# Performance work log

Measured on AMD Instinct MI355X. Metric: run time of the kernel, lower is better.

The kernel has to match this reference:

```python
import jax, jax.numpy as jnp
import numpy as np


def gin_conv(x, src, dst, W, b, num_nodes):
    # PyG GINConv with eps=0: nn((1+eps)*x + sum_{j in N(i)} x_j)
    agg = jax.ops.segment_sum(x[src], dst, num_segments=num_nodes)
    return (x + agg) @ W + b


def setup_inputs() -> dict:
    key = jax.random.key(0)
    ks = jax.random.split(key, 16)
    N, E, F, G = 100000, 3200000, 64, 512
    x = jax.random.normal(ks[0], (N, F), dtype=jnp.float32)
    edge_index = jax.random.randint(ks[1], (2, E), 0, N, dtype=jnp.int64)
    batch = jnp.sort(jax.random.randint(ks[2], (N,), 0, G, dtype=jnp.int64))

    def lin(k, fi, fo):
        return jax.random.normal(k, (fi, fo), dtype=jnp.float32) / np.sqrt(fi)

    return {
        "x": x, "edge_index": edge_index, "batch": batch, "num_graphs": G,
        "W1": lin(ks[3], F, 32), "b1": jnp.zeros((32,), jnp.float32),
        "W2": lin(ks[4], 32, 64), "b2": jnp.zeros((64,), jnp.float32),
        "W3": lin(ks[5], 64, 64), "b3": jnp.zeros((64,), jnp.float32),
        "Wf1": lin(ks[6], 64, 64), "bf1": jnp.zeros((64,), jnp.float32),
        "Wf2": lin(ks[7], 64, 32), "bf2": jnp.zeros((32,), jnp.float32),
        "Wf3": lin(ks[8], 32, 1), "bf3": jnp.zeros((1,), jnp.float32),
    }


def reference(x, edge_index, batch, num_graphs,
              W1, b1, W2, b2, W3, b3, Wf1, bf1, Wf2, bf2, Wf3, bf3):
    N = x.shape[0]
    src, dst = edge_index[0], edge_index[1]
    h = jax.nn.elu(gin_conv(x, src, dst, W1, b1, N))
    h = jax.nn.elu(gin_conv(h, src, dst, W2, b2, N))
    h = jax.nn.elu(gin_conv(h, src, dst, W3, b3, N))
    # scatter_mean pooling over graphs
    sums = jax.ops.segment_sum(h, batch, num_segments=num_graphs)
    cnts = jax.ops.segment_sum(jnp.ones((N,), h.dtype), batch, num_segments=num_graphs)
    g = sums / jnp.maximum(cnts, 1.0)[:, None]
    g = jax.nn.elu(g @ Wf1 + bf1)
    g = jax.nn.elu(g @ Wf2 + bf2)
    g = g @ Wf3 + bf3
    return g.reshape(-1)
```

## Files before the change

kernel.cpp:

```cpp
#include <hip/hip_runtime.h>
#include <hip/hip_bf16.h>


typedef float f4 __attribute__((ext_vector_type(4)));

#define NCHUNK 512
#define MAXK 1024

__device__ __forceinline__ float elu_f(float x) {
  return x > 0.0f ? x : expm1f(x);
}

__device__ __forceinline__ float rl(float v, int q) {
  return __int_as_float(__builtin_amdgcn_readlane(__float_as_int(v), q));
}

__device__ __forceinline__ unsigned short f2bf(float f) {
  unsigned int u = __float_as_uint(f);
  u = (u + 0x7FFFu + ((u >> 16) & 1u)) >> 16;
  return (unsigned short)u;
}

__device__ __forceinline__ void acc_add8(float* a, const uint4 w) {
  a[0] += __uint_as_float(w.x << 16);
  a[1] += __uint_as_float(w.x & 0xffff0000u);
  a[2] += __uint_as_float(w.y << 16);
  a[3] += __uint_as_float(w.y & 0xffff0000u);
  a[4] += __uint_as_float(w.z << 16);
  a[5] += __uint_as_float(w.z & 0xffff0000u);
  a[6] += __uint_as_float(w.w << 16);
  a[7] += __uint_as_float(w.w & 0xffff0000u);
}


__global__ __launch_bounds__(256) void cvt_bf16_kernel(
    const float* __restrict__ in, unsigned short* __restrict__ out, int n4) {
  typedef unsigned short us4 __attribute__((ext_vector_type(4)));
  const int stride = gridDim.x * blockDim.x;
  for (int i = blockIdx.x * blockDim.x + threadIdx.x; i < n4; i += stride) {
    const f4 v = *reinterpret_cast<const f4*>(in + (long long)i * 4);
    us4 o;
    o.x = f2bf(v.x); o.y = f2bf(v.y); o.z = f2bf(v.z); o.w = f2bf(v.w);
    *reinterpret_cast<us4*>(out + (long long)i * 4) = o;
  }
}


__global__ __launch_bounds__(256) void bucket_hist_kernel(
    const int* __restrict__ dst, int* __restrict__ bhist, int E, int K, int chunk) {
  __shared__ int h[MAXK];
  for (int k = threadIdx.x; k < K; k += 256) h[k] = 0;
  __syncthreads();
  const int base = blockIdx.x * chunk;
  const int end = min(E, base + chunk);
  for (int e = base + threadIdx.x; e < end; e += 256)
    atomicAdd(&h[dst[e] >> 7], 1);
  __syncthreads();
  int* row = bhist + (long long)blockIdx.x * K;
  for (int k = threadIdx.x; k < K; k += 256) row[k] = h[k];
}

__global__ __launch_bounds__(NCHUNK) void chunk_scan_kernel(
    const int* __restrict__ bhist, int* __restrict__ cursors,
    int* __restrict__ btot, int K) {
  __shared__ int s[NCHUNK];
  const int k = blockIdx.x;
  const int t = threadIdx.x;
  const int own = bhist[(long long)t * K + k];
  s[t] = own;
  __syncthreads();
#pragma unroll
  for (int off = 1; off < NCHUNK; off <<= 1) {
    int v = (t >= off) ? s[t - off] : 0;
    __syncthreads();
    s[t] += v;
    __syncthreads();
  }
  cursors[(long long)t * K + k] = s[t] - own;
  if (t == NCHUNK - 1) btot[k] = s[t];
}

__global__ __launch_bounds__(1024) void bucket_scan_kernel(
    const int* __restrict__ btot, int* __restrict__ bstart, int K) {
  __shared__ int s[1024];
  const int t = threadIdx.x;
  const int own = (t < K) ? btot[t] : 0;
  s[t] = own;
  __syncthreads();
#pragma unroll
  for (int off = 1; off < 1024; off <<= 1) {
    int v = (t >= off) ? s[t - off] : 0;
    __syncthreads();
    s[t] += v;
    __syncthreads();
  }
  if (t < K) bstart[t] = s[t] - own;
  if (t == K - 1) bstart[K] = s[t];
}

__global__ __launch_bounds__(256) void bucket_scatter_kernel(
    const int* __restrict__ src, const int* __restrict__ dst,
    const int* __restrict__ cursors, const int* __restrict__ bstart,
    int* __restrict__ packed, int E, int K, int chunk) {
  __shared__ int cur[MAXK];
  const int c = blockIdx.x;
  for (int k = threadIdx.x; k < K; k += 256)
    cur[k] = cursors[(long long)c * K + k] + bstart[k];
  __syncthreads();
  const int base = c * chunk;
  const int end = min(E, base + chunk);
  for (int e = base + threadIdx.x; e < end; e += 256) {
    const int d = dst[e];
    const int k = d >> 7;
    const int p = atomicAdd(&cur[k], 1);
    packed[p] = ((d & 127) << 18) | src[e];
  }
}

__global__ __launch_bounds__(256) void bucket_sort_kernel(
    const int* __restrict__ packed, const int* __restrict__ bstart,
    int* __restrict__ rowptr, int* __restrict__ eidx, int N, int E, int K) {
  __shared__ int hcnt[128];
  __shared__ int sc[128];
  __shared__ int ccur[128];
  const int k = blockIdx.x;
  const int t = threadIdx.x;
  const int n0 = k << 7;
  const int e0 = bstart[k];
  const int e1 = bstart[k + 1];
  if (t < 128) hcnt[t] = 0;
  __syncthreads();
  for (int e = e0 + t; e < e1; e += 256)
    atomicAdd(&hcnt[packed[e] >> 18], 1);
  __syncthreads();
  if (t < 128) sc[t] = hcnt[t];
  __syncthreads();
#pragma unroll
  for (int off = 1; off < 128; off <<= 1) {
    int v = 0;
    if (t < 128 && t >= off) v = sc[t - off];
    __syncthreads();
    if (t < 128) sc[t] += v;
    __syncthreads();
  }
  if (t < 128) {
    const int excl = sc[t] - hcnt[t];
    ccur[t] = excl;
    if (n0 + t < N) rowptr[n0 + t] = e0 + excl;
  }
  if (k == 0 && t == 0) rowptr[N] = E;
  __syncthreads();
  for (int e = e0 + t; e < e1; e += 256) {
    const int w = packed[e];
    const int dl = w >> 18;
    const int p = atomicAdd(&ccur[dl], 1);
    eidx[e0 + p] = w & 0x3FFFF;
  }
}


template <int FO>
__global__ __launch_bounds__(256) void gin_layer64_kernel(
    const unsigned short* __restrict__ h, const int* __restrict__ rowptr,
    const int* __restrict__ eidx, const float* __restrict__ W,
    const float* __restrict__ b, unsigned short* __restrict__ out, int N) {
  const int lane = threadIdx.x & 63;
  const int grp = lane >> 3;
  const int li = lane & 7;
  const int wid = blockIdx.x * (blockDim.x >> 6) + (threadIdx.x >> 6);
  const int nw = gridDim.x * (blockDim.x >> 6);
  const int fo = lane & (FO - 1);
  float wcol[64];
#pragma unroll
  for (int k = 0; k < 64; ++k) wcol[k] = W[k * FO + fo];
  const float bias = b[fo];

  for (int n = wid; n < N; n += nw) {
    const int r0 = rowptr[n];
    const int cnt = rowptr[n + 1] - r0;
    float a[8] = {0.f, 0.f, 0.f, 0.f, 0.f, 0.f, 0.f, 0.f};
    int i = grp;
    for (; i + 8 < cnt; i += 16) {
      const int s0 = eidx[r0 + i];
      const int s1 = eidx[r0 + i + 8];
      const uint4 w0 = *reinterpret_cast<const uint4*>(h + (long long)s0 * 64 + li * 8);
      const uint4 w1 = *reinterpret_cast<const uint4*>(h + (long long)s1 * 64 + li * 8);
      acc_add8(a, w0);
      acc_add8(a, w1);
    }
    if (i < cnt) {
      const int s = eidx[r0 + i];
      acc_add8(a, *reinterpret_cast<const uint4*>(h + (long long)s * 64 + li * 8));
    }
#pragma unroll
    for (int j = 0; j < 8; ++j) {
      a[j] += __shfl_xor(a[j], 8, 64);
      a[j] += __shfl_xor(a[j], 16, 64);
      a[j] += __shfl_xor(a[j], 32, 64);
    }
    acc_add8(a, *reinterpret_cast<const uint4*>(h + (long long)n * 64 + li * 8));
    float o0 = bias, o1 = 0.0f;
#pragma unroll
    for (int k = 0; k < 64; k += 2) {
      o0 = fmaf(rl(a[k & 7], k >> 3), wcol[k], o0);
      o1 = fmaf(rl(a[(k + 1) & 7], (k + 1) >> 3), wcol[k + 1], o1);
    }
    if (lane < FO) out[(long long)n * FO + lane] = f2bf(elu_f(o0 + o1));
  }
}

__global__ __launch_bounds__(256) void gin_layer32_kernel(
    const unsigned short* __restrict__ h, const int* __restrict__ rowptr,
    const int* __restrict__ eidx, const float* __restrict__ W,
    const float* __restrict__ b, unsigned short* __restrict__ out, int N) {
  const int lane = threadIdx.x & 63;
  const int grp = lane >> 2;
  const int li = lane & 3;
  const int wid = blockIdx.x * (blockDim.x >> 6) + (threadIdx.x >> 6);
  const int nw = gridDim.x * (blockDim.x >> 6);
  float wcol[32];
#pragma unroll
  for (int k = 0; k < 32; ++k) wcol[k] = W[k * 64 + lane];
  const float bias = b[lane];

  for (int n = wid; n < N; n += nw) {
    const int r0 = rowptr[n];
    const int cnt = rowptr[n + 1] - r0;
    float a[8] = {0.f, 0.f, 0.f, 0.f, 0.f, 0.f, 0.f, 0.f};
    int i = grp;
    for (; i + 16 < cnt; i += 32) {
      const int s0 = eidx[r0 + i];
      const int s1 = eidx[r0 + i + 16];
      const uint4 w0 = *reinterpret_cast<const uint4*>(h + (long long)s0 * 32 + li * 8);
      const uint4 w1 = *reinterpret_cast<const uint4*>(h + (long long)s1 * 32 + li * 8);
      acc_add8(a, w0);
      acc_add8(a, w1);
    }
    if (i < cnt) {
      const int s = eidx[r0 + i];
      acc_add8(a, *reinterpret_cast<const uint4*>(h + (long long)s * 32 + li * 8));
    }
#pragma unroll
    for (int j = 0; j < 8; ++j) {
      a[j] += __shfl_xor(a[j], 4, 64);
      a[j] += __shfl_xor(a[j], 8, 64);
      a[j] += __shfl_xor(a[j], 16, 64);
      a[j] += __shfl_xor(a[j], 32, 64);
    }
    acc_add8(a, *reinterpret_cast<const uint4*>(h + (long long)n * 32 + li * 8));
    float o0 = bias, o1 = 0.0f;
#pragma unroll
    for (int k = 0; k < 32; k += 2) {
      o0 = fmaf(rl(a[k & 7], k >> 3), wcol[k], o0);
      o1 = fmaf(rl(a[(k + 1) & 7], (k + 1) >> 3), wcol[k + 1], o1);
    }
    out[(long long)n * 64 + lane] = f2bf(elu_f(o0 + o1));
  }
}


__global__ void pool_kernel(const unsigned short* __restrict__ h,
                            const int* __restrict__ batch,
                            float* __restrict__ sums,
                            float* __restrict__ cnts,
                            int N) {
  const int groupsPerBlock = blockDim.x >> 6;
  const int grp = blockIdx.x * groupsPerBlock + (threadIdx.x >> 6);
  const int ngrp = gridDim.x * groupsPerBlock;
  const int f = threadIdx.x & 63;
  const int chunk = (N + ngrp - 1) / ngrp;
  const int n0 = grp * chunk;
  const int n1 = min(N, n0 + chunk);
  if (n0 >= n1) return;
  int g = batch[n0];
  float acc = 0.0f;
  float cnt = 0.0f;
  for (int n = n0; n < n1; ++n) {
    const int bg = batch[n];
    if (bg != g) {
      atomicAdd(&sums[(long long)g * 64 + f], acc);
      if (f == 0) atomicAdd(&cnts[g], cnt);
      acc = 0.0f;
      cnt = 0.0f;
      g = bg;
    }
    acc += __uint_as_float((unsigned int)h[(long long)n * 64 + f] << 16);
    cnt += 1.0f;
  }
  atomicAdd(&sums[(long long)g * 64 + f], acc);
  if (f == 0) atomicAdd(&cnts[g], cnt);
}

__global__ void head_kernel(const float* __restrict__ sums,
                            const float* __restrict__ cnts,
                            const float* __restrict__ Wf1, const float* __restrict__ bf1,
                            const float* __restrict__ Wf2, const float* __restrict__ bf2,
                            const float* __restrict__ Wf3, const float* __restrict__ bf3,
                            float* __restrict__ out, int G) {
  __shared__ float s0[64];
  __shared__ float s1[64];
  __shared__ float s2[32];
  const int g = blockIdx.x;
  const int t = threadIdx.x;
  const float c = fmaxf(cnts[g], 1.0f);
  s0[t] = sums[(long long)g * 64 + t] / c;
  __syncthreads();
  float acc = bf1[t];
#pragma unroll
  for (int k = 0; k < 64; ++k) acc += s0[k] * Wf1[k * 64 + t];
  s1[t] = elu_f(acc);
  __syncthreads();
  if (t < 32) {
    float a2 = bf2[t];
#pragma unroll
    for (int k = 0; k < 64; ++k) a2 += s1[k] * Wf2[k * 32 + t];
    s2[t] = elu_f(a2) * Wf3[t];
  }
  __syncthreads();
  if (t == 0) {
    float r = bf3[0];
#pragma unroll
    for (int k = 0; k < 32; ++k) r += s2[k];
    out[g] = r;
  }
}

extern "C" void kernel_launch(void* const* d_in, const int* in_sizes, int n_in,
                              void* d_out, int out_size, void* d_ws, size_t ws_size,
                              hipStream_t stream) {
  const float* x   = (const float*)d_in[0];
  const int* ei    = (const int*)d_in[1];
  const int* batch = (const int*)d_in[2];
  const float* W1  = (const float*)d_in[4];
  const float* b1  = (const float*)d_in[5];
  const float* W2  = (const float*)d_in[6];
  const float* b2  = (const float*)d_in[7];
  const float* W3  = (const float*)d_in[8];
  const float* b3  = (const float*)d_in[9];
  const float* Wf1 = (const float*)d_in[10];
  const float* bf1 = (const float*)d_in[11];
  const float* Wf2 = (const float*)d_in[12];
  const float* bf2 = (const float*)d_in[13];
  const float* Wf3 = (const float*)d_in[14];
  const float* bf3 = (const float*)d_in[15];

  const int N = in_sizes[0] / 64;
  const int E = in_sizes[1] / 2;
  const int G = out_size;
  const int* src = ei;
  const int* dst = ei + E;
  const int K = (N + 127) >> 7;
  const int chunk = (E + NCHUNK - 1) / NCHUNK;

  char* ws = (char*)d_ws;
  size_t off = 0;
  auto alloc = [&](size_t bytes) -> void* {
    void* p = ws + off;
    off = (off + bytes + 255) & ~(size_t)255;
    return p;
  };
  int* bhist   = (int*)alloc((size_t)NCHUNK * K * 4);
  int* cursors = (int*)alloc((size_t)NCHUNK * K * 4);
  int* btot    = (int*)alloc((size_t)K * 4);
  int* bstart  = (int*)alloc((size_t)(K + 1) * 4);
  int* rowptr  = (int*)alloc((size_t)(N + 1) * 4);
  int* eidx    = (int*)alloc((size_t)E * 4);
  int* packed  = (int*)alloc((size_t)E * 4);
  unsigned short* xb = (unsigned short*)alloc((size_t)N * 64 * 2);
  unsigned short* hA = (unsigned short*)alloc((size_t)N * 64 * 2);
  unsigned short* hB = (unsigned short*)alloc((size_t)N * 64 * 2);
  float* sums  = (float*)alloc((size_t)G * 64 * 4);
  float* cnts  = (float*)alloc((size_t)G * 4);
  float* out   = (float*)d_out;

  cvt_bf16_kernel<<<1024, 256, 0, stream>>>(x, xb, N * 16);

  bucket_hist_kernel<<<NCHUNK, 256, 0, stream>>>(dst, bhist, E, K, chunk);
  chunk_scan_kernel<<<K, NCHUNK, 0, stream>>>(bhist, cursors, btot, K);
  bucket_scan_kernel<<<1, 1024, 0, stream>>>(btot, bstart, K);
  bucket_scatter_kernel<<<NCHUNK, 256, 0, stream>>>(src, dst, cursors, bstart,
                                                    packed, E, K, chunk);
  bucket_sort_kernel<<<K, 256, 0, stream>>>(packed, bstart, rowptr, eidx, N, E, K);

  gin_layer64_kernel<32><<<2048, 256, 0, stream>>>(xb, rowptr, eidx, W1, b1, hA, N);
  gin_layer32_kernel<<<2048, 256, 0, stream>>>(hA, rowptr, eidx, W2, b2, hB, N);
  gin_layer64_kernel<64><<<2048, 256, 0, stream>>>(hB, rowptr, eidx, W3, b3, hA, N);

  hipMemsetAsync(sums, 0, (size_t)G * 64 * 4, stream);
  hipMemsetAsync(cnts, 0, (size_t)G * 4, stream);
  pool_kernel<<<512, 256, 0, stream>>>(hA, batch, sums, cnts, N);
  head_kernel<<<G, 64, 0, stream>>>(sums, cnts, Wf1, bf1, Wf2, bf2, Wf3, bf3, out, G);
}
```

Measured before the change: 473.7 us.

## Use wave-shuffle scans, dual accumulators, split-K FO=32 matmul, merged memset

Replaces the shared-memory Hillis-Steele scans in chunk_scan and bucket_sort with wavefront shuffle scans plus a small cross-wave fixup, cutting block barriers. The gather loops in the GIN layers use two independent accumulator sets to break the add dependency chain. The FO=32 layer splits the 64-wide K dimension across the two half-waves using ds_bpermute, then reduces with a shuffle, so all 64 lanes do useful FMAs. The two pooling memsets are merged into one by placing the counts right after the sums.

```diff
diff --git a/kernel.cpp b/kernel.cpp
--- a/kernel.cpp
+++ b/kernel.cpp
@@ -63,21 +63,30 @@
 __global__ __launch_bounds__(NCHUNK) void chunk_scan_kernel(
     const int* __restrict__ bhist, int* __restrict__ cursors,
     int* __restrict__ btot, int K) {
-  __shared__ int s[NCHUNK];
   const int k = blockIdx.x;
   const int t = threadIdx.x;
+  const int lane = t & 63;
+  const int wv = t >> 6;
   const int own = bhist[(long long)t * K + k];
-  s[t] = own;
-  __syncthreads();
-#pragma unroll
-  for (int off = 1; off < NCHUNK; off <<= 1) {
-    int v = (t >= off) ? s[t - off] : 0;
-    __syncthreads();
-    s[t] += v;
-    __syncthreads();
-  }
-  cursors[(long long)t * K + k] = s[t] - own;
-  if (t == NCHUNK - 1) btot[k] = s[t];
+  int v = own;
+#pragma unroll
+  for (int off = 1; off < 64; off <<= 1) {
+    int u = __shfl_up(v, off, 64);
+    if (lane >= off) v += u;
+  }
+  __shared__ int wsum[8];
+  __shared__ int wpre[8];
+  if (lane == 63) wsum[wv] = v;
+  __syncthreads();
+  if (t == 0) {
+    int p = 0;
+#pragma unroll
+    for (int w = 0; w < 8; ++w) { wpre[w] = p; p += wsum[w]; }
+  }
+  __syncthreads();
+  v += wpre[wv];
+  cursors[(long long)t * K + k] = v - own;
+  if (t == NCHUNK - 1) btot[k] = v;
 }
 
 __global__ __launch_bounds__(1024) void bucket_scan_kernel(
@@ -121,10 +130,11 @@
     const int* __restrict__ packed, const int* __restrict__ bstart,
     int* __restrict__ rowptr, int* __restrict__ eidx, int N, int E, int K) {
   __shared__ int hcnt[128];
-  __shared__ int sc[128];
   __shared__ int ccur[128];
+  __shared__ int wtot;
   const int k = blockIdx.x;
   const int t = threadIdx.x;
+  const int lane = t & 63;
   const int n0 = k << 7;
   const int e0 = bstart[k];
   const int e1 = bstart[k + 1];
@@ -133,18 +143,21 @@
   for (int e = e0 + t; e < e1; e += 256)
     atomicAdd(&hcnt[packed[e] >> 18], 1);
   __syncthreads();
-  if (t < 128) sc[t] = hcnt[t];
-  __syncthreads();
-#pragma unroll
-  for (int off = 1; off < 128; off <<= 1) {
-    int v = 0;
-    if (t < 128 && t >= off) v = sc[t - off];
-    __syncthreads();
-    if (t < 128) sc[t] += v;
-    __syncthreads();
-  }
+  int v = 0, own = 0;
   if (t < 128) {
-    const int excl = sc[t] - hcnt[t];
+    own = hcnt[t];
+    v = own;
+#pragma unroll
+    for (int off = 1; off < 64; off <<= 1) {
+      int u = __shfl_up(v, off, 64);
+      if (lane >= off) v += u;
+    }
+  }
+  if (t == 63) wtot = v;
+  __syncthreads();
+  if (t >= 64 && t < 128) v += wtot;
+  if (t < 128) {
+    const int excl = v - own;
     ccur[t] = excl;
     if (n0 + t < N) rowptr[n0 + t] = e0 + excl;
   }
@@ -170,15 +183,22 @@
   const int wid = blockIdx.x * (blockDim.x >> 6) + (threadIdx.x >> 6);
   const int nw = gridDim.x * (blockDim.x >> 6);
   const int fo = lane & (FO - 1);
-  float wcol[64];
-#pragma unroll
-  for (int k = 0; k < 64; ++k) wcol[k] = W[k * FO + fo];
+  float wcol[(FO == 32) ? 32 : 64];
+  if constexpr (FO == 32) {
+    const int kbase = (lane >> 5) * 32;
+#pragma unroll
+    for (int j = 0; j < 32; ++j) wcol[j] = W[(kbase + j) * 32 + fo];
+  } else {
+#pragma unroll
+    for (int k = 0; k < 64; ++k) wcol[k] = W[k * 64 + fo];
+  }
   const float bias = b[fo];
 
   for (int n = wid; n < N; n += nw) {
     const int r0 = rowptr[n];
     const int cnt = rowptr[n + 1] - r0;
     float a[8] = {0.f, 0.f, 0.f, 0.f, 0.f, 0.f, 0.f, 0.f};
+    float a2[8] = {0.f, 0.f, 0.f, 0.f, 0.f, 0.f, 0.f, 0.f};
     int i = grp;
     for (; i + 8 < cnt; i += 16) {
       const int s0 = eidx[r0 + i];
@@ -186,7 +206,7 @@
       const uint4 w0 = *reinterpret_cast<const uint4*>(h + (long long)s0 * 64 + li * 8);
       const uint4 w1 = *reinterpret_cast<const uint4*>(h + (long long)s1 * 64 + li * 8);
       acc_add8(a, w0);
-      acc_add8(a, w1);
+      acc_add8(a2, w1);
     }
     if (i < cnt) {
       const int s = eidx[r0 + i];
@@ -194,18 +214,32 @@
     }
 #pragma unroll
     for (int j = 0; j < 8; ++j) {
+      a[j] += a2[j];
       a[j] += __shfl_xor(a[j], 8, 64);
       a[j] += __shfl_xor(a[j], 16, 64);
       a[j] += __shfl_xor(a[j], 32, 64);
     }
     acc_add8(a, *reinterpret_cast<const uint4*>(h + (long long)n * 64 + li * 8));
-    float o0 = bias, o1 = 0.0f;
-#pragma unroll
-    for (int k = 0; k < 64; k += 2) {
-      o0 = fmaf(rl(a[k & 7], k >> 3), wcol[k], o0);
-      o1 = fmaf(rl(a[(k + 1) & 7], (k + 1) >> 3), wcol[k + 1], o1);
-    }
-    if (lane < FO) out[(long long)n * FO + lane] = f2bf(elu_f(o0 + o1));
+    if constexpr (FO == 32) {
+      float o = (lane < 32) ? bias : 0.0f;
+      const int pbase = (lane >> 5) * 16;
+#pragma unroll
+      for (int j = 0; j < 32; ++j) {
+        const float av = __int_as_float(__builtin_amdgcn_ds_bpermute(
+            pbase + (j >> 3) * 4, __float_as_int(a[j & 7])));
+        o = fmaf(av, wcol[j], o);
+      }
+      o += __shfl_xor(o, 32, 64);
+      if (lane < 32) out[(long long)n * 32 + lane] = f2bf(elu_f(o));
+    } else {
+      float o0 = bias, o1 = 0.0f;
+#pragma unroll
+      for (int k = 0; k < 64; k += 2) {
+        o0 = fmaf(rl(a[k & 7], k >> 3), wcol[k], o0);
+        o1 = fmaf(rl(a[(k + 1) & 7], (k + 1) >> 3), wcol[k + 1], o1);
+      }
+      out[(long long)n * 64 + lane] = f2bf(elu_f(o0 + o1));
+    }
   }
 }
 
@@ -227,6 +261,7 @@
     const int r0 = rowptr[n];
     const int cnt = rowptr[n + 1] - r0;
     float a[8] = {0.f, 0.f, 0.f, 0.f, 0.f, 0.f, 0.f, 0.f};
+    float a2[8] = {0.f, 0.f, 0.f, 0.f, 0.f, 0.f, 0.f, 0.f};
     int i = grp;
     for (; i + 16 < cnt; i += 32) {
       const int s0 = eidx[r0 + i];
@@ -234,7 +269,7 @@
       const uint4 w0 = *reinterpret_cast<const uint4*>(h + (long long)s0 * 32 + li * 8);
       const uint4 w1 = *reinterpret_cast<const uint4*>(h + (long long)s1 * 32 + li * 8);
       acc_add8(a, w0);
-      acc_add8(a, w1);
+      acc_add8(a2, w1);
     }
     if (i < cnt) {
       const int s = eidx[r0 + i];
@@ -242,6 +277,7 @@
     }
 #pragma unroll
     for (int j = 0; j < 8; ++j) {
+      a[j] += a2[j];
       a[j] += __shfl_xor(a[j], 4, 64);
       a[j] += __shfl_xor(a[j], 8, 64);
       a[j] += __shfl_xor(a[j], 16, 64);
@@ -369,8 +405,8 @@
   unsigned short* xb = (unsigned short*)alloc((size_t)N * 64 * 2);
   unsigned short* hA = (unsigned short*)alloc((size_t)N * 64 * 2);
   unsigned short* hB = (unsigned short*)alloc((size_t)N * 64 * 2);
-  float* sums  = (float*)alloc((size_t)G * 64 * 4);
-  float* cnts  = (float*)alloc((size_t)G * 4);
+  float* sums  = (float*)alloc((size_t)G * 65 * 4);
+  float* cnts  = sums + (size_t)G * 64;
   float* out   = (float*)d_out;
 
   cvt_bf16_kernel<<<1024, 256, 0, stream>>>(x, xb, N * 16);
@@ -386,8 +422,7 @@
   gin_layer32_kernel<<<2048, 256, 0, stream>>>(hA, rowptr, eidx, W2, b2, hB, N);
   gin_layer64_kernel<64><<<2048, 256, 0, stream>>>(hB, rowptr, eidx, W3, b3, hA, N);
 
-  hipMemsetAsync(sums, 0, (size_t)G * 64 * 4, stream);
-  hipMemsetAsync(cnts, 0, (size_t)G * 4, stream);
+  hipMemsetAsync(sums, 0, (size_t)G * 65 * 4, stream);
   pool_kernel<<<512, 256, 0, stream>>>(hA, batch, sums, cnts, N);
   head_kernel<<<G, 64, 0, stream>>>(sums, cnts, Wf1, bf1, Wf2, bf2, Wf3, bf3, out, G);
 }
```

Result: no change. 477.1 us (+0.7%).
